# Kernel optimization log

Hardware: AMD Instinct MI355X
Metric: run time of the kernel (lower is better)

Reference implementation:

```python
import jax, jax.numpy as jnp
import numpy as np

H = 256  # hidden_dim
B = 256  # batch
T = 512  # seq_len


def setup_inputs() -> dict:
    key = jax.random.key(0)
    ks = jax.random.split(key, 16)
    s_in = 1.0  # torch LSTMCell init: U(-1/sqrt(H), 1/sqrt(H)); use scaled normal for simplicity
    sc = 1.0 / np.sqrt(H)
    inp = {
        "input": jax.random.normal(ks[0], (B, T), dtype=jnp.float32),
        # layer 1: input_size = 1
        "W_ih1": jax.random.uniform(ks[1], (4 * H, 1), jnp.float32, -sc, sc),
        "W_hh1": jax.random.uniform(ks[2], (4 * H, H), jnp.float32, -sc, sc),
        "b_ih1": jax.random.uniform(ks[3], (4 * H,), jnp.float32, -sc, sc),
        "b_hh1": jax.random.uniform(ks[4], (4 * H,), jnp.float32, -sc, sc),
        # layer 2
        "W_ih2": jax.random.uniform(ks[5], (4 * H, H), jnp.float32, -sc, sc),
        "W_hh2": jax.random.uniform(ks[6], (4 * H, H), jnp.float32, -sc, sc),
        "b_ih2": jax.random.uniform(ks[7], (4 * H,), jnp.float32, -sc, sc),
        "b_hh2": jax.random.uniform(ks[8], (4 * H,), jnp.float32, -sc, sc),
        # layer 3
        "W_ih3": jax.random.uniform(ks[9], (4 * H, H), jnp.float32, -sc, sc),
        "W_hh3": jax.random.uniform(ks[10], (4 * H, H), jnp.float32, -sc, sc),
        "b_ih3": jax.random.uniform(ks[11], (4 * H,), jnp.float32, -sc, sc),
        "b_hh3": jax.random.uniform(ks[12], (4 * H,), jnp.float32, -sc, sc),
        # output head Linear(H, 1)
        "W_lin": jax.random.uniform(ks[13], (1, H), jnp.float32, -sc, sc),
        "b_lin": jax.random.uniform(ks[14], (1,), jnp.float32, -sc, sc),
    }
    return inp


def _lstm_cell(x, h, c, Wi, Wh, bi, bh):
    # PyTorch LSTMCell gate order: i, f, g, o
    gates = x @ Wi.T + bi + h @ Wh.T + bh  # [B, 4H]
    i, f, g, o = jnp.split(gates, 4, axis=-1)
    c_new = jax.nn.sigmoid(f) * c + jax.nn.sigmoid(i) * jnp.tanh(g)
    h_new = jax.nn.sigmoid(o) * jnp.tanh(c_new)
    return h_new, c_new


def reference(input, W_ih1, W_hh1, b_ih1, b_hh1, W_ih2, W_hh2, b_ih2, b_hh2,
              W_ih3, W_hh3, b_ih3, b_hh3, W_lin, b_lin):
    n = input.shape[0]
    z = jnp.zeros((n, H), dtype=jnp.float32)
    init = (z, z, z, z, z, z)  # (h1, c1, h2, c2, h3, c3)
    xs = input.T[:, :, None]  # [T, B, 1]

    def step(carry, x_t):
        h1, c1, h2, c2, h3, c3 = carry
        h1, c1 = _lstm_cell(x_t, h1, c1, W_ih1, W_hh1, b_ih1, b_hh1)
        h2, c2 = _lstm_cell(h1, h2, c2, W_ih2, W_hh2, b_ih2, b_hh2)
        h3, c3 = _lstm_cell(h2, h3, c3, W_ih3, W_hh3, b_ih3, b_hh3)
        y = h3 @ W_lin.T + b_lin  # [B, 1] (dropout p=0 is identity)
        return (h1, c1, h2, c2, h3, c3), y

    _, ys = jax.lax.scan(step, init, xs)  # ys: [T, B, 1]
    return ys[:, :, 0].T  # [B, T], matches torch.cat(outputs, dim=1)
```

## Files before the change

kernel.cpp:

```cpp
#include <hip/hip_runtime.h>
#include <stdint.h>


#define Hd 256
#define Bd 256
#define Td 512
#define RING 4
#define GH 8
#define GB 8
#define CPAD 32

typedef __attribute__((ext_vector_type(8))) short short8;
typedef __attribute__((ext_vector_type(4))) float floatx4;
typedef __attribute__((ext_vector_type(4))) unsigned int uintx4;

__device__ __forceinline__ unsigned short f2bf(float f) {
  union { float f; unsigned int u; } v; v.f = f;
  return (unsigned short)((v.u + 0x7fffu + ((v.u >> 16) & 1u)) >> 16);
}
__device__ __forceinline__ float sigm(float x) { return 1.0f / (1.0f + __expf(-x)); }
__device__ __forceinline__ float tanhfast(float x) { return 2.0f / (1.0f + __expf(-2.0f * x)) - 1.0f; }

__device__ __forceinline__ void spin_relaxed(unsigned int* p, unsigned int v) {
  while (__hip_atomic_load(p, __ATOMIC_RELAXED, __HIP_MEMORY_SCOPE_AGENT) < v) { }
}

__global__ __launch_bounds__(512, 2) void lstm3_kernel(
    const float* __restrict__ xin,
    const float* __restrict__ Wi1, const float* __restrict__ Wh1,
    const float* __restrict__ bi1, const float* __restrict__ bh1,
    const float* __restrict__ Wi2, const float* __restrict__ Wh2,
    const float* __restrict__ bi2, const float* __restrict__ bh2,
    const float* __restrict__ Wi3, const float* __restrict__ Wh3,
    const float* __restrict__ bi3, const float* __restrict__ bh3,
    const float* __restrict__ Wlin, const float* __restrict__ blin,
    float* __restrict__ out,
    unsigned int* __restrict__ cnt,
    unsigned short* __restrict__ ring)
{
  __shared__ float gl[4][32][33];
  __shared__ uintx4 hbuf[2][1024];

  const int bid = blockIdx.x;
  const int j   = bid / 24;
  const int rem = bid - j * 24;
  const int l   = rem >> 3;
  const int g   = rem & 7;

  const int tid  = threadIdx.x;
  const int lane = tid & 63;
  const int wave = tid >> 6;
  const int tau  = wave & 3;
  const int mh   = wave >> 2;
  const int quad = lane >> 4;
  const int l15  = lane & 15;

  const int ubase = j * 32;
  const int rbase = g * 32;

  const float* Wpi = (l == 1) ? Wi2 : Wi3;
  const float* Wph = (l == 0) ? Wh1 : ((l == 1) ? Wh2 : Wh3);
  const float* bi  = (l == 0) ? bi1 : ((l == 1) ? bi2 : bi3);
  const float* bh  = (l == 0) ? bh1 : ((l == 1) ? bh2 : bh3);

  short8 breg[2][16];
  {
    const int koff = quad * 8;
    #pragma unroll
    for (int nt = 0; nt < 2; ++nt) {
      const int grow = tau * Hd + ubase + nt * 16 + l15;
      #pragma unroll
      for (int kc = 0; kc < 16; ++kc) {
        short8 v = {0, 0, 0, 0, 0, 0, 0, 0};
        const float* src = nullptr;
        if (kc < 8) { if (l != 0) src = Wpi + (size_t)grow * Hd + kc * 32 + koff; }
        else        { src = Wph + (size_t)grow * Hd + (kc - 8) * 32 + koff; }
        if (src) {
          #pragma unroll
          for (int e = 0; e < 8; ++e) v[e] = (short)f2bf(src[e]);
        }
        breg[nt][kc] = v;
      }
    }
  }

  const int clrow = tid >> 4;
  const int cu0   = (tid & 15) * 2;
  float bsum[4][2], wiv[4][2], wlv[2];
  #pragma unroll
  for (int tt = 0; tt < 4; ++tt) {
    #pragma unroll
    for (int du = 0; du < 2; ++du) {
      const int gg = tt * Hd + ubase + cu0 + du;
      bsum[tt][du] = bi[gg] + bh[gg];
      wiv[tt][du]  = (l == 0) ? Wi1[gg] : 0.0f;
    }
  }
  wlv[0] = (l == 2) ? Wlin[ubase + cu0]     : 0.0f;
  wlv[1] = (l == 2) ? Wlin[ubase + cu0 + 1] : 0.0f;
  const float bl0 = (l == 2 && j == 0) ? blin[0] : 0.0f;

  float cst0 = 0.0f, cst1 = 0.0f;

  unsigned int* myC = cnt + (l * GB + g) * CPAD;
  unsigned int* upC = cnt + ((l - 1) * GB + g) * CPAD;
  unsigned int* dnC = cnt + ((l + 1) * GB + g) * CPAD;
  unsigned short* ownR = ring + (size_t)l * RING * Bd * Hd;
  const unsigned short* upRb = ring + (size_t)(l - 1) * RING * Bd * Hd;

  const float* xrow = xin + (size_t)(rbase + clrow) * Td;

  const int c0 = tid;
  const int c1 = tid + 512;
  const int o0 = (tid & 31) * 512 + (tid >> 7) * 64 + ((tid >> 5) & 3) * 16;
  const int o1 = o0 + 256;
  const int fragbase = quad * 32 + mh * 16 + l15;

  {
    uintx4 z = {0u, 0u, 0u, 0u};
    hbuf[1][c0] = z;
    hbuf[1][c1] = z;
  }

  for (int t = 0; t < Td; ++t) {
    {
      bool active = false; unsigned int* p = nullptr; unsigned need = 0;
      if (tid == 0)      { active = (t > 0);                p = myC; need = GH * t; }
      else if (tid == 1) { active = (l > 0);                p = upC; need = GH * (t + 1); }
      else if (tid == 2) { active = (l < 2) && (t >= RING); p = dnC; need = GH * (t - RING + 1); }
      if (active) spin_relaxed(p, need);
    }
    __syncthreads();

    uintx4 u0, u1, v0, v1;
    if (l != 0) {
      const char* upReg = (const char*)(upRb + (size_t)(t & (RING - 1)) * Bd * Hd
                                        + (size_t)rbase * Hd);
      asm volatile("global_load_dwordx4 %0, %1, off sc0 sc1"
                   : "=&v"(u0) : "v"(upReg + o0));
      asm volatile("global_load_dwordx4 %0, %1, off sc0 sc1"
                   : "=&v"(u1) : "v"(upReg + o1));
    }
    if (t != 0) {
      const char* ownReg = (const char*)(ownR + (size_t)((t + RING - 1) & (RING - 1)) * Bd * Hd
                                         + (size_t)rbase * Hd);
      asm volatile("global_load_dwordx4 %0, %1, off sc0 sc1"
                   : "=&v"(v0) : "v"(ownReg + o0));
      asm volatile("global_load_dwordx4 %0, %1, off sc0 sc1"
                   : "=&v"(v1) : "v"(ownReg + o1));
    }
    asm volatile("s_waitcnt vmcnt(0)" ::: "memory");
    if (l != 0) { hbuf[0][c0] = u0; hbuf[0][c1] = u1; }
    if (t != 0) { hbuf[1][c0] = v0; hbuf[1][c1] = v1; }
    __syncthreads();

    short8 av[16];
    if (l != 0) {
      #pragma unroll
      for (int kc = 0; kc < 8; ++kc)
        av[kc] = *reinterpret_cast<const short8*>(&hbuf[0][kc * 128 + fragbase]);
    }
    #pragma unroll
    for (int kc = 0; kc < 8; ++kc)
      av[8 + kc] = *reinterpret_cast<const short8*>(&hbuf[1][kc * 128 + fragbase]);

    floatx4 acc0 = {0.f, 0.f, 0.f, 0.f};
    floatx4 acc1 = {0.f, 0.f, 0.f, 0.f};
    if (l != 0) {
      #pragma unroll
      for (int kc = 0; kc < 8; ++kc) {
        acc0 = __builtin_amdgcn_mfma_f32_16x16x32_bf16(av[kc], breg[0][kc], acc0, 0, 0, 0);
        acc1 = __builtin_amdgcn_mfma_f32_16x16x32_bf16(av[kc], breg[1][kc], acc1, 0, 0, 0);
      }
    }
    #pragma unroll
    for (int kc = 8; kc < 16; ++kc) {
      acc0 = __builtin_amdgcn_mfma_f32_16x16x32_bf16(av[kc], breg[0][kc], acc0, 0, 0, 0);
      acc1 = __builtin_amdgcn_mfma_f32_16x16x32_bf16(av[kc], breg[1][kc], acc1, 0, 0, 0);
    }

    {
      const int lr = mh * 16 + quad * 4;
      #pragma unroll
      for (int r2 = 0; r2 < 4; ++r2) {
        gl[tau][lr + r2][l15]      = acc0[r2];
        gl[tau][lr + r2][16 + l15] = acc1[r2];
      }
    }
    __syncthreads();

    float h0, h1;
    {
      const float xv = (l == 0) ? xrow[t] : 0.0f;
      float pi = gl[0][clrow][cu0] + bsum[0][0] + xv * wiv[0][0];
      float pf = gl[1][clrow][cu0] + bsum[1][0] + xv * wiv[1][0];
      float pg = gl[2][clrow][cu0] + bsum[2][0] + xv * wiv[2][0];
      float po = gl[3][clrow][cu0] + bsum[3][0] + xv * wiv[3][0];
      float ii = sigm(pi), ff = sigm(pf), gv = tanhfast(pg), oo = sigm(po);
      cst0 = ff * cst0 + ii * gv;
      h0 = oo * tanhfast(cst0);
      pi = gl[0][clrow][cu0 + 1] + bsum[0][1] + xv * wiv[0][1];
      pf = gl[1][clrow][cu0 + 1] + bsum[1][1] + xv * wiv[1][1];
      pg = gl[2][clrow][cu0 + 1] + bsum[2][1] + xv * wiv[2][1];
      po = gl[3][clrow][cu0 + 1] + bsum[3][1] + xv * wiv[3][1];
      ii = sigm(pi); ff = sigm(pf); gv = tanhfast(pg); oo = sigm(po);
      cst1 = ff * cst1 + ii * gv;
      h1 = oo * tanhfast(cst1);
    }

    {
      unsigned short* dst = ownR + (size_t)(t & (RING - 1)) * Bd * Hd
                          + (size_t)(rbase + clrow) * Hd + ubase + cu0;
      const unsigned int packed = (unsigned int)f2bf(h0) | ((unsigned int)f2bf(h1) << 16);
      __hip_atomic_store((unsigned int*)dst, packed, __ATOMIC_RELAXED,
                         __HIP_MEMORY_SCOPE_AGENT);
    }

    if (l == 2) {
      float pr = wlv[0] * h0 + wlv[1] * h1;
      pr += __shfl_xor(pr, 8);
      pr += __shfl_xor(pr, 4);
      pr += __shfl_xor(pr, 2);
      pr += __shfl_xor(pr, 1);
      if ((tid & 15) == 0) {
        atomicAdd(&out[(size_t)(rbase + clrow) * Td + t], pr + bl0);
      }
    }

    __syncthreads();
    if (tid == 0) {
      __hip_atomic_fetch_add(myC, 1u, __ATOMIC_RELAXED, __HIP_MEMORY_SCOPE_AGENT);
    }
  }
}

extern "C" void kernel_launch(void* const* d_in, const int* in_sizes, int n_in,
                              void* d_out, int out_size, void* d_ws, size_t ws_size,
                              hipStream_t stream) {
  const float* xin  = (const float*)d_in[0];
  const float* Wi1  = (const float*)d_in[1];
  const float* Wh1  = (const float*)d_in[2];
  const float* bi1  = (const float*)d_in[3];
  const float* bh1  = (const float*)d_in[4];
  const float* Wi2  = (const float*)d_in[5];
  const float* Wh2  = (const float*)d_in[6];
  const float* bi2  = (const float*)d_in[7];
  const float* bh2  = (const float*)d_in[8];
  const float* Wi3  = (const float*)d_in[9];
  const float* Wh3  = (const float*)d_in[10];
  const float* bi3  = (const float*)d_in[11];
  const float* bh3  = (const float*)d_in[12];
  const float* Wlin = (const float*)d_in[13];
  const float* blin = (const float*)d_in[14];
  float* out = (float*)d_out;

  unsigned int*   cnt  = (unsigned int*)d_ws;
  unsigned short* ring = (unsigned short*)((char*)d_ws + 4096);

  hipMemsetAsync(d_ws, 0, 4096, stream);
  hipMemsetAsync(d_out, 0, (size_t)out_size * sizeof(float), stream);

  lstm3_kernel<<<dim3(3 * GB * GH), dim3(512), 0, stream>>>(
      xin, Wi1, Wh1, bi1, bh1, Wi2, Wh2, bi2, bh2,
      Wi3, Wh3, bi3, bh3, Wlin, blin, out, cnt, ring);
}
```

Before: 1.916 ms.

## Use per-block step flags instead of shared atomic counters, swizzle LDS fragment layout

```diff
diff --git a/kernel.cpp b/kernel.cpp
--- a/kernel.cpp
+++ b/kernel.cpp
@@ -8,7 +8,7 @@
 #define RING 4
 #define GH 8
 #define GB 8
-#define CPAD 32
+#define GPAD 32
 
 typedef __attribute__((ext_vector_type(8))) short short8;
 typedef __attribute__((ext_vector_type(4))) float floatx4;
@@ -102,19 +102,21 @@
 
   float cst0 = 0.0f, cst1 = 0.0f;
 
-  unsigned int* myC = cnt + (l * GB + g) * CPAD;
-  unsigned int* upC = cnt + ((l - 1) * GB + g) * CPAD;
-  unsigned int* dnC = cnt + ((l + 1) * GB + g) * CPAD;
+  unsigned int* myS = cnt + (l * GB + g) * GPAD;
+  unsigned int* upS = cnt + ((l - 1) * GB + g) * GPAD;
+  unsigned int* dnS = cnt + ((l + 1) * GB + g) * GPAD;
   unsigned short* ownR = ring + (size_t)l * RING * Bd * Hd;
   const unsigned short* upRb = ring + (size_t)(l - 1) * RING * Bd * Hd;
 
   const float* xrow = xin + (size_t)(rbase + clrow) * Td;
 
-  const int c0 = tid;
-  const int c1 = tid + 512;
-  const int o0 = (tid & 31) * 512 + (tid >> 7) * 64 + ((tid >> 5) & 3) * 16;
-  const int o1 = o0 + 256;
-  const int fragbase = quad * 32 + mh * 16 + l15;
+  const int o0 = tid * 16;
+  const int o1 = o0 + 8192;
+  const int kc0 = (tid >> 2) & 7, q0 = tid & 3, row0 = tid >> 5;
+  const int c0 = kc0 * 128 + q0 * 32 + (row0 ^ (q0 | ((kc0 & 1) << 2)));
+  const int c1 = c0 + 16;
+  const int fragEven = quad * 32 + mh * 16 + (l15 ^ quad);
+  const int fragOdd  = quad * 32 + mh * 16 + (l15 ^ (quad | 4));
 
   {
     uintx4 z = {0u, 0u, 0u, 0u};
@@ -125,9 +127,9 @@
   for (int t = 0; t < Td; ++t) {
     {
       bool active = false; unsigned int* p = nullptr; unsigned need = 0;
-      if (tid == 0)      { active = (t > 0);                p = myC; need = GH * t; }
-      else if (tid == 1) { active = (l > 0);                p = upC; need = GH * (t + 1); }
-      else if (tid == 2) { active = (l < 2) && (t >= RING); p = dnC; need = GH * (t - RING + 1); }
+      if (tid < 8)       { active = (t > 0);                p = myS + tid;        need = t; }
+      else if (tid < 16) { active = (l > 0);                p = upS + (tid - 8);  need = t + 1; }
+      else if (tid < 24) { active = (l < 2) && (t >= RING); p = dnS + (tid - 16); need = t - RING + 1; }
       if (active) spin_relaxed(p, need);
     }
     __syncthreads();
@@ -158,11 +160,13 @@
     if (l != 0) {
       #pragma unroll
       for (int kc = 0; kc < 8; ++kc)
-        av[kc] = *reinterpret_cast<const short8*>(&hbuf[0][kc * 128 + fragbase]);
+        av[kc] = *reinterpret_cast<const short8*>(
+            &hbuf[0][kc * 128 + ((kc & 1) ? fragOdd : fragEven)]);
     }
     #pragma unroll
     for (int kc = 0; kc < 8; ++kc)
-      av[8 + kc] = *reinterpret_cast<const short8*>(&hbuf[1][kc * 128 + fragbase]);
+      av[8 + kc] = *reinterpret_cast<const short8*>(
+          &hbuf[1][kc * 128 + ((kc & 1) ? fragOdd : fragEven)]);
 
     floatx4 acc0 = {0.f, 0.f, 0.f, 0.f};
     floatx4 acc1 = {0.f, 0.f, 0.f, 0.f};
@@ -229,7 +233,8 @@
 
     __syncthreads();
     if (tid == 0) {
-      __hip_atomic_fetch_add(myC, 1u, __ATOMIC_RELAXED, __HIP_MEMORY_SCOPE_AGENT);
+      __hip_atomic_store(myS + j, (unsigned int)(t + 1), __ATOMIC_RELAXED,
+                         __HIP_MEMORY_SCOPE_AGENT);
     }
   }
 }
```

New measurement: 1.898 ms. Within noise of the previous version (-0.9%).
